# Kernel tuning notes

Measured on AMD Instinct MI355X. Metric: run time of the kernel, lower is better.

The kernel has to match this reference:

```python
import jax, jax.numpy as jnp
import numpy as np

N_QUBITS = 14
N_LAYERS = 3
BATCH = 256


def _apply_1q(state, U, q, n):
    # state: (B, 2^n) flat; apply 2x2 gate U on qubit q.
    # U: (2,2) shared or (B,2,2) per-sample.
    B = state.shape[0]
    s = state.reshape(B, 2 ** q, 2, 2 ** (n - 1 - q))
    if U.ndim == 3:
        s = jnp.einsum('bij,bajc->baic', U, s)
    else:
        s = jnp.einsum('ij,bajc->baic', U, s)
    return s.reshape(B, -1)


def _apply_cnot(state, c, t, n):
    # CNOT: |c, t> -> |c, t xor c>. Flip target axis on the control=1 block.
    B = state.shape[0]
    a, b = (c, t) if c < t else (t, c)
    s = state.reshape(B, 2 ** a, 2, 2 ** (b - a - 1), 2, 2 ** (n - 1 - b))
    c_ax = 2 if c < t else 4
    t_ax = 4 if c < t else 2
    s0 = jax.lax.index_in_dim(s, 0, axis=c_ax, keepdims=False)
    s1 = jax.lax.index_in_dim(s, 1, axis=c_ax, keepdims=False)
    t_ax2 = t_ax if t_ax < c_ax else t_ax - 1
    s1 = jnp.flip(s1, axis=t_ax2)
    s = jnp.stack([s0, s1], axis=c_ax)
    return s.reshape(B, -1)


def _circuit(x, weights, n, L):
    # angles constrained to (-pi, pi) as in the torch wrapper
    angles = jnp.tanh(x) * jnp.float32(np.pi)  # (B, n)
    B = x.shape[0]
    state = jnp.zeros((B, 2 ** n), jnp.complex64).at[:, 0].set(1.0)
    # AngleEmbedding with RY rotations (per-sample gate matrices)
    for q in range(n):
        th = angles[:, q] * 0.5
        c, s = jnp.cos(th), jnp.sin(th)
        U = jnp.stack([jnp.stack([c, -s], -1), jnp.stack([s, c], -1)], -2)
        state = _apply_1q(state, U.astype(jnp.complex64), q, n)
    # BasicEntanglerLayers: per layer, RX(w) on each wire then CNOT ring
    for l in range(L):
        for q in range(n):
            th = weights[l, q] * 0.5
            c = jnp.cos(th).astype(jnp.complex64)
            s = jnp.sin(th).astype(jnp.complex64)
            mis = jnp.complex64(-1j) * s
            U = jnp.stack([jnp.stack([c, mis]), jnp.stack([mis, c])])
            state = _apply_1q(state, U, q, n)
        num_cnots = n if n > 2 else (1 if n == 2 else 0)
        for q in range(num_cnots):
            state = _apply_cnot(state, q, (q + 1) % n, n)
    # <Z_q> = P(q=0) - P(q=1)
    p = (jnp.abs(state) ** 2).reshape((B,) + (2,) * n)  # float32 probs
    expvals = []
    for q in range(n):
        pq = jnp.sum(p, axis=tuple(a for a in range(1, n + 1) if a != q + 1))
        expvals.append(pq[:, 0] - pq[:, 1])
    return jnp.stack(expvals, axis=-1)  # (B, n)


def setup_inputs() -> dict:
    key = jax.random.key(0)
    kx, kw = jax.random.split(key)
    x = jax.random.normal(kx, (BATCH, N_QUBITS), jnp.float32)
    # TorchLayer default init for BasicEntanglerLayers: uniform in [0, 2*pi)
    weights = jax.random.uniform(kw, (N_LAYERS, N_QUBITS), jnp.float32, 0.0, 2.0 * np.pi)
    return {"x": x, "weights": weights}


def reference(x, weights):
    return _circuit(x, weights, N_QUBITS, N_LAYERS)
```

## Files before the change

kernel.cpp:

```cpp
#include <hip/hip_runtime.h>
#include <math.h>

#define NQ 14
#define DIM (1 << NQ)
#define NT 512
#define TA 32
#define NW (NT / 64)
#define PDIM (DIM + DIM / 32)

template <int J> struct IC { static constexpr int v = J; };
template <int N, typename F>
__device__ __forceinline__ void sfor(F&& f) {
    if constexpr (N > 0) { sfor<N - 1>(f); f(IC<N - 1>{}); }
}

typedef float cf2 __attribute__((ext_vector_type(2)));

__device__ __forceinline__ cf2 pk_mul_s_swapneg(cf2 cs, cf2 a) {
    cf2 t;
    asm("v_pk_mul_f32 %0, %1, %2 op_sel:[1,1] op_sel_hi:[1,0] neg_hi:[0,1]"
        : "=v"(t) : "v"(cs), "v"(a));
    return t;
}
__device__ __forceinline__ cf2 pk_fma_c(cf2 cs, cf2 a, cf2 b) {
    cf2 d;
    asm("v_pk_fma_f32 %0, %1, %2, %3 op_sel:[0,0,0] op_sel_hi:[0,1,1]"
        : "=v"(d) : "v"(cs), "v"(a), "v"(b));
    return d;
}

struct St {
    cf2 a0, a1, a2, a3, a4, a5, a6, a7, a8, a9, a10, a11, a12, a13, a14, a15,
        a16, a17, a18, a19, a20, a21, a22, a23, a24, a25, a26, a27, a28, a29, a30, a31;
};
template <int J> __device__ __forceinline__ cf2& amp(St& s);
#define AMP_GET(J) template <> __device__ __forceinline__ cf2& amp<J>(St& s) { return s.a##J; }
AMP_GET(0)  AMP_GET(1)  AMP_GET(2)  AMP_GET(3)  AMP_GET(4)  AMP_GET(5)  AMP_GET(6)  AMP_GET(7)
AMP_GET(8)  AMP_GET(9)  AMP_GET(10) AMP_GET(11) AMP_GET(12) AMP_GET(13) AMP_GET(14) AMP_GET(15)
AMP_GET(16) AMP_GET(17) AMP_GET(18) AMP_GET(19) AMP_GET(20) AMP_GET(21) AMP_GET(22) AMP_GET(23)
AMP_GET(24) AMP_GET(25) AMP_GET(26) AMP_GET(27) AMP_GET(28) AMP_GET(29) AMP_GET(30) AMP_GET(31)

__host__ __device__ constexpr int pad(int idx) { return idx + (idx >> 5); }

template <int P0, int P1, int P2, int P3, int P4>
struct Tile5 {
    static constexpr int PMASK = (1 << P0) | (1 << P1) | (1 << P2) | (1 << P3) | (1 << P4);
    static __device__ __forceinline__ int base_idx(int t) {
        int idx = 0, tb = 0;
#pragma unroll
        for (int p = 0; p < NQ; ++p)
            if (!((PMASK >> p) & 1)) { idx |= ((t >> tb) & 1) << p; ++tb; }
        return idx;
    }
    static constexpr int off(int j) {
        return ((j & 1) << P0) | (((j >> 1) & 1) << P1) | (((j >> 2) & 1) << P2) |
               (((j >> 3) & 1) << P3) | (((j >> 4) & 1) << P4);
    }
    static constexpr int poff(int j) { return pad(off(j)); }
};
template <int P0, int P1, int P2, int P3, int P4,
          int Q0, int Q1, int Q2, int Q3, int Q4, int Q5, int Q6, int Q7, int Q8>
struct Tile5Q {
    static __device__ __forceinline__ int base_idx(int t) {
        return (((t >> 0) & 1) << Q0) | (((t >> 1) & 1) << Q1) | (((t >> 2) & 1) << Q2) |
               (((t >> 3) & 1) << Q3) | (((t >> 4) & 1) << Q4) | (((t >> 5) & 1) << Q5) |
               (((t >> 6) & 1) << Q6) | (((t >> 7) & 1) << Q7) | (((t >> 8) & 1) << Q8);
    }
    static constexpr int off(int j) {
        return ((j & 1) << P0) | (((j >> 1) & 1) << P1) | (((j >> 2) & 1) << P2) |
               (((j >> 3) & 1) << P3) | (((j >> 4) & 1) << P4);
    }
    static constexpr int poff(int j) { return pad(off(j)); }
};

using TT1 = Tile5<9, 10, 11, 12, 13>;
using TT2Q = Tile5Q<4, 5, 6, 7, 8,  9, 0, 1, 2, 3, 10, 11, 12, 13>;
using TT3 = Tile5<13, 0, 1, 2, 3>;

template <class T>
__device__ __forceinline__ void load_tile_fold(const cf2* s, int pbLo, int pbHi, St& st) {
    sfor<TA>([&](auto jc) {
        constexpr int j0 = decltype(jc)::v;
        constexpr int j = (j0 >> 1) | ((j0 & 1) << 4);
        amp<j>(st) = s[((j & 16) ? pbHi : pbLo) + T::poff(j)];
    });
}
template <class T, int HI>
__device__ __forceinline__ void store_half(cf2* s, int pb, St& st) {
    sfor<TA>([&](auto jc) {
        constexpr int j = decltype(jc)::v;
        if constexpr ((j >> 4) == HI) s[pb + T::poff(j)] = amp<j>(st);
    });
}

template <int LB>
__device__ __forceinline__ void g_rx(St& st, cf2 cs) {
    sfor<TA>([&](auto jc) {
        constexpr int j = decltype(jc)::v;
        if constexpr (!(j & (1 << LB))) {
            constexpr int k = j | (1 << LB);
            cf2 aj = amp<j>(st), ak = amp<k>(st);
            amp<j>(st) = pk_fma_c(cs, aj, pk_mul_s_swapneg(cs, ak));
            amp<k>(st) = pk_fma_c(cs, ak, pk_mul_s_swapneg(cs, aj));
        }
    });
}
template <int LB, int HI>
__device__ __forceinline__ void g_rx_h(St& st, cf2 cs) {
    sfor<TA>([&](auto jc) {
        constexpr int j = decltype(jc)::v;
        if constexpr (!(j & (1 << LB)) && ((j >> 4) == HI)) {
            constexpr int k = j | (1 << LB);
            cf2 aj = amp<j>(st), ak = amp<k>(st);
            amp<j>(st) = pk_fma_c(cs, aj, pk_mul_s_swapneg(cs, ak));
            amp<k>(st) = pk_fma_c(cs, ak, pk_mul_s_swapneg(cs, aj));
        }
    });
}
template <int CTRL>
__device__ __forceinline__ void g_rx_lane_dpp(St& st, cf2 cs) {
    sfor<TA>([&](auto jc) {
        constexpr int j = decltype(jc)::v;
        cf2 a = amp<j>(st);
        int px = __builtin_amdgcn_update_dpp(__float_as_int(a.x), __float_as_int(a.x),
                                             CTRL, 0xF, 0xF, false);
        int py = __builtin_amdgcn_update_dpp(__float_as_int(a.y), __float_as_int(a.y),
                                             CTRL, 0xF, 0xF, false);
        cf2 p; p.x = __int_as_float(px); p.y = __int_as_float(py);
        amp<j>(st) = pk_fma_c(cs, a, pk_mul_s_swapneg(cs, p));
    });
}
template <int LC, int LT, int HI>
__device__ __forceinline__ void g_cnot_h(St& st) {
    sfor<TA>([&](auto jc) {
        constexpr int j = decltype(jc)::v;
        if constexpr (((j >> LC) & 1) && !((j >> LT) & 1) && ((j >> 4) == HI)) {
            constexpr int k = j | (1 << LT);
            cf2 t = amp<j>(st);
            amp<j>(st) = amp<k>(st);
            amp<k>(st) = t;
        }
    });
}

__device__ __forceinline__ cf2 cmul(cf2 a, cf2 b) {
    cf2 r; r.x = a.x * b.x - a.y * b.y; r.y = a.x * b.y + a.y * b.x; return r;
}
__device__ __forceinline__ cf2 v_of(cf2 ry, cf2 rx, int b) {
    cf2 r;
    r.x = b ? rx.x * ry.y : rx.x * ry.x;
    r.y = b ? -(rx.y * ry.x) : -(rx.y * ry.y);
    return r;
}

template <int CTRL, int RM>
__device__ __forceinline__ float dpp_add_step(float v) {
    int t = __builtin_amdgcn_update_dpp(0, __float_as_int(v), CTRL, RM, 0xF, true);
    return v + __int_as_float(t);
}
__device__ __forceinline__ float wave_red(float v) {
    v = dpp_add_step<0x111, 0xF>(v);
    v = dpp_add_step<0x112, 0xF>(v);
    v = dpp_add_step<0x114, 0xF>(v);
    v = dpp_add_step<0x118, 0xF>(v);
    v = dpp_add_step<0x142, 0xA>(v);
    v = dpp_add_step<0x143, 0xC>(v);
    return v;
}

__global__ void __launch_bounds__(NT) qsim_kernel(const float* __restrict__ x,
                                                  const float* __restrict__ w,
                                                  float* __restrict__ out) {
    __shared__ cf2 sSt[PDIM];
    __shared__ cf2 sCS[56];
    __shared__ float sRed[NW][NQ];

    const int tid = threadIdx.x;
    const int b = blockIdx.x;

    if (tid < 56) {
        float f;
        if (tid < 14) {
            float v = x[b * NQ + tid];
            float e = __builtin_amdgcn_exp2f(v * 2.8853900817779268f);
            float t = fmaf(-2.f, __builtin_amdgcn_rcpf(e + 1.f), 1.f);
            f = t * 0.25f;
        } else {
            f = w[tid - 14] * 0.07957747154594767f;
        }
        cf2 v2; v2.x = __builtin_amdgcn_cosf(f); v2.y = __builtin_amdgcn_sinf(f);
        sCS[tid] = v2;
    }

    const int pbT1 = pad(TT1::base_idx(tid));
    const int pbT2 = pad(TT2Q::base_idx(tid));
    const int pbT3 = pad(TT3::base_idx(tid));
    const int d2 = (tid & 1) ? 264 : 0;
    const int pbT2lo = pbT2 + d2, pbT2hi = pbT2 - d2;
    const int d3 = (tid & 1) ? 8 : 0;
    const int pbT3lo = pbT3 + d3, pbT3hi = pbT3 - d3;

    __syncthreads();

    St st;

    {
        const int t0 = tid & 1,        t1 = (tid >> 1) & 1, t2 = (tid >> 2) & 1,
                  t3 = (tid >> 3) & 1, t4 = (tid >> 4) & 1, t5 = (tid >> 5) & 1,
                  t6 = (tid >> 6) & 1, t7 = (tid >> 7) & 1, t8 = (tid >> 8) & 1;
        const int b6 = t7 ^ t8, b7 = t6 ^ t7, b8 = t5 ^ t6, b9 = t4 ^ t5;
        const int b10 = t3 ^ t4, b11 = t2 ^ t3, b12 = t1 ^ t2, b13 = t0 ^ t1;
        cf2 Pref = v_of(sCS[6], sCS[20], b6);
        Pref = cmul(Pref, v_of(sCS[7],  sCS[21], b7));
        Pref = cmul(Pref, v_of(sCS[8],  sCS[22], b8));
        Pref = cmul(Pref, v_of(sCS[9],  sCS[23], b9));
        Pref = cmul(Pref, v_of(sCS[10], sCS[24], b10));
        Pref = cmul(Pref, v_of(sCS[11], sCS[25], b11));
        Pref = cmul(Pref, v_of(sCS[12], sCS[26], b12));
        Pref = cmul(Pref, v_of(sCS[13], sCS[27], b13));
        cf2 w0[2] = { v_of(sCS[0], sCS[14], t0),     v_of(sCS[0], sCS[14], 1 ^ t0) };
        cf2 w1[2] = { v_of(sCS[1], sCS[15], t0),     v_of(sCS[1], sCS[15], 1 ^ t0) };
        cf2 v2[2] = { v_of(sCS[2], sCS[16], 0),      v_of(sCS[2], sCS[16], 1) };
        cf2 v3[2] = { v_of(sCS[3], sCS[17], 0),      v_of(sCS[3], sCS[17], 1) };
        cf2 v4[2] = { v_of(sCS[4], sCS[18], 0),      v_of(sCS[4], sCS[18], 1) };
        cf2 w5[2] = { v_of(sCS[5], sCS[19], t8),     v_of(sCS[5], sCS[19], 1 ^ t8) };
        cf2 u[4] = { cmul(v4[0], w5[0]), cmul(v4[1], w5[1]),
                     cmul(v4[1], w5[0]), cmul(v4[0], w5[1]) };
        cf2 tA[2], tB[4], tC[8], tD[16];
        sfor<2>([&](auto ic) {
            constexpr int i = decltype(ic)::v;
            tA[i] = cmul(Pref, w0[i]);
        });
        sfor<4>([&](auto ic) {
            constexpr int i = decltype(ic)::v;
            constexpr int j4 = i >> 1, j3 = i & 1;
            tB[i] = cmul(tA[j4], w1[j3 ^ j4]);
        });
        sfor<8>([&](auto ic) {
            constexpr int i = decltype(ic)::v;
            constexpr int j3 = (i >> 1) & 1, j2 = i & 1;
            tC[i] = cmul(tB[i >> 1], v2[j2 ^ j3]);
        });
        sfor<16>([&](auto ic) {
            constexpr int i = decltype(ic)::v;
            constexpr int j2 = (i >> 1) & 1, j1 = i & 1;
            tD[i] = cmul(tC[i >> 1], v3[j1 ^ j2]);
        });
        sfor<TA>([&](auto jc) {
            constexpr int j = decltype(jc)::v;
            constexpr int j0 = j & 1, j1 = (j >> 1) & 1;
            amp<j>(st) = cmul(tD[j >> 1], u[(j1 << 1) | j0]);
        });

        g_rx<4>(st, sCS[28 + 0]);
        g_rx_h<3, 0>(st, sCS[28 + 1]); g_rx_h<2, 0>(st, sCS[28 + 2]);
        g_rx_h<1, 0>(st, sCS[28 + 3]); g_rx_h<0, 0>(st, sCS[28 + 4]);
        g_cnot_h<3, 2, 0>(st); g_cnot_h<2, 1, 0>(st); g_cnot_h<1, 0, 0>(st);
        g_rx_h<3, 0>(st, sCS[42 + 1]); g_rx_h<2, 0>(st, sCS[42 + 2]);
        g_rx_h<1, 0>(st, sCS[42 + 3]);
        store_half<TT1, 0>(sSt, pbT1, st);
        g_rx_h<3, 1>(st, sCS[28 + 1]); g_rx_h<2, 1>(st, sCS[28 + 2]);
        g_rx_h<1, 1>(st, sCS[28 + 3]); g_rx_h<0, 1>(st, sCS[28 + 4]);
        g_cnot_h<4, 3, 1>(st); g_cnot_h<3, 2, 1>(st); g_cnot_h<2, 1, 1>(st); g_cnot_h<1, 0, 1>(st);
        g_rx_h<3, 1>(st, sCS[42 + 1]); g_rx_h<2, 1>(st, sCS[42 + 2]);
        g_rx_h<1, 1>(st, sCS[42 + 3]);
        store_half<TT1, 1>(sSt, pbT1, st);
    }
    __syncthreads();

    {
        cf2 c5 = sCS[28 + 5], c6 = sCS[28 + 6], c7 = sCS[28 + 7];
        cf2 c8 = sCS[28 + 8], c9 = sCS[28 + 9];
        cf2 e4 = sCS[42 + 4], e5 = sCS[42 + 5], e6 = sCS[42 + 6];
        cf2 e7 = sCS[42 + 7], e8 = sCS[42 + 8];
        load_tile_fold<TT2Q>(sSt, pbT2lo, pbT2hi, st);
        g_rx<4>(st, c5);
        g_rx_lane_dpp<0xB1>(st, e4);
        g_rx_h<3,0>(st, c6); g_rx_h<2,0>(st, c7); g_rx_h<1,0>(st, c8); g_rx_h<0,0>(st, c9);
        g_cnot_h<3,2,0>(st); g_cnot_h<2,1,0>(st); g_cnot_h<1,0,0>(st);
        g_rx_h<3,1>(st, c6); g_rx_h<2,1>(st, c7); g_rx_h<1,1>(st, c8); g_rx_h<0,1>(st, c9);
        g_cnot_h<4,3,1>(st); g_cnot_h<3,2,1>(st); g_cnot_h<2,1,1>(st); g_cnot_h<1,0,1>(st);
        g_rx<4>(st, e5);
        g_rx_h<3,0>(st, e6); g_rx_h<2,0>(st, e7); g_rx_h<1,0>(st, e8);
        store_half<TT2Q, 0>(sSt, pbT2, st);
        g_rx_h<3,1>(st, e6); g_rx_h<2,1>(st, e7); g_rx_h<1,1>(st, e8);
        store_half<TT2Q, 1>(sSt, pbT2, st);
    }
    __syncthreads();

    {
        cf2 cA = sCS[28 + 10], cB = sCS[28 + 11], cC = sCS[28 + 12], cD = sCS[28 + 13];
        cf2 eA = sCS[42 + 10], eB = sCS[42 + 11], eC = sCS[42 + 12], eD = sCS[42 + 13];
        cf2 e9 = sCS[42 + 9],  e0 = sCS[42 + 0];
        load_tile_fold<TT3>(sSt, pbT3lo, pbT3hi, st);
        g_rx<4>(st, cA);
        g_rx_lane_dpp<0xB1>(st, e9);
        g_rx_h<3,0>(st, cB); g_rx_h<2,0>(st, cC); g_rx_h<1,0>(st, cD);
        g_cnot_h<3,2,0>(st); g_cnot_h<2,1,0>(st); g_cnot_h<1,0,0>(st);
        g_rx_h<3,1>(st, cB); g_rx_h<2,1>(st, cC); g_rx_h<1,1>(st, cD);
        g_cnot_h<4,3,1>(st); g_cnot_h<3,2,1>(st); g_cnot_h<2,1,1>(st); g_cnot_h<1,0,1>(st);
        g_rx<4>(st, eA);
        g_rx_h<3,0>(st, eB); g_rx_h<2,0>(st, eC); g_rx_h<1,0>(st, eD); g_rx_h<0,0>(st, e0);
        g_rx_h<3,1>(st, eB); g_rx_h<2,1>(st, eC); g_rx_h<1,1>(st, eD); g_rx_h<0,1>(st, e0);
    }

    {
        float Aa = 0.f, Ab = 0.f, Ac = 0.f, Ad = 0.f, Ae = 0.f, Af = 0.f;
        sfor<TA>([&](auto jc) {
            constexpr int j = decltype(jc)::v;
            cf2 v = amp<j>(st);
            float pj = v.x * v.x + v.y * v.y;
            constexpr int j0 = j & 1, j1 = (j >> 1) & 1, j2 = (j >> 2) & 1,
                          j3 = (j >> 3) & 1, j4 = (j >> 4) & 1;
            constexpr int sa = j0;
            constexpr int sb = j0 ^ j4;
            constexpr int sc = sb ^ j3;
            constexpr int sd = sc ^ j2;
            constexpr int se = sd ^ j1;
            constexpr int sf = se ^ j0;
            Aa += sa ? -pj : pj;
            Ab += sb ? -pj : pj;
            Ac += sc ? -pj : pj;
            Ad += sd ? -pj : pj;
            Ae += se ? -pj : pj;
            Af += sf ? -pj : pj;
        });
        const int t0 = tid & 1,        t1 = (tid >> 1) & 1, t2 = (tid >> 2) & 1,
                  t3 = (tid >> 3) & 1, t4 = (tid >> 4) & 1, t5 = (tid >> 5) & 1,
                  t6 = (tid >> 6) & 1, t7 = (tid >> 7) & 1, t8 = (tid >> 8) & 1;
        const int L4 = t5, L5 = L4 ^ t4, L6 = L5 ^ t3;
        const int L7 = L6 ^ t2, L8 = L7 ^ t1, L9 = L8 ^ t0;
        const int W1 = t8, W2 = W1 ^ t7, W3 = W2 ^ t6;

        float R0 = wave_red(Aa);
        float R4 = wave_red(L4 ? -Aa : Aa);
        float R5 = wave_red(L5 ? -Aa : Aa);
        float R6 = wave_red(L6 ? -Aa : Aa);
        float R7 = wave_red(L7 ? -Aa : Aa);
        float R8 = wave_red(L8 ? -Aa : Aa);
        float R9 = wave_red(L9 ? -Aa : Aa);
        float RB = wave_red(L9 ? -Ab : Ab);
        float RC = wave_red(L9 ? -Ac : Ac);
        float RD = wave_red(L9 ? -Ad : Ad);
        float RE = wave_red(L9 ? -Ae : Ae);
        float RF = wave_red(L9 ? -Af : Af);

        const int wv = tid >> 6, ln = tid & 63;
        if (ln == 63) {
            sRed[wv][0]  = W3 ? -RF : RF;
            sRed[wv][1]  = W1 ? -R0 : R0;
            sRed[wv][2]  = W2 ? -R0 : R0;
            sRed[wv][3]  = W3 ? -R0 : R0;
            sRed[wv][4]  = W3 ? -R4 : R4;
            sRed[wv][5]  = W3 ? -R5 : R5;
            sRed[wv][6]  = W3 ? -R6 : R6;
            sRed[wv][7]  = W3 ? -R7 : R7;
            sRed[wv][8]  = W3 ? -R8 : R8;
            sRed[wv][9]  = W3 ? -R9 : R9;
            sRed[wv][10] = W3 ? -RB : RB;
            sRed[wv][11] = W3 ? -RC : RC;
            sRed[wv][12] = W3 ? -RD : RD;
            sRed[wv][13] = W3 ? -RE : RE;
        }
        __syncthreads();
        if (tid < NQ) {
            float acc = 0.f;
#pragma unroll
            for (int k = 0; k < NW; ++k) acc += sRed[k][tid];
            out[b * NQ + tid] = acc;
        }
    }
}

extern "C" void kernel_launch(void* const* d_in, const int* in_sizes, int n_in,
                              void* d_out, int out_size, void* d_ws, size_t ws_size,
                              hipStream_t stream) {
    const float* x = (const float*)d_in[0];
    const float* w = (const float*)d_in[1];
    float* out = (float*)d_out;
    qsim_kernel<<<256, NT, 0, stream>>>(x, w, out);
}
```

Measured before the change: 67.87 us.

## Double threads per block with 16-amplitude register tiles and DPP cross-lane gates

Raises the block size from 512 to 1024 threads and halves each thread's register tile from 32 to 16 amplitudes. All three LDS tile layouts, the product-state initialisation and the reduction sign bookkeeping are redefined for the new split. More gates and CNOTs that now cross lanes are done with DPP lane swaps (quad_perm patterns) instead of in-register pairs, and the half-tile staging of the old version is dropped. The intent is more parallelism and lower register pressure per thread, at the cost of extra DPP traffic, more wave reductions per block and a larger block to synchronise.

```diff
diff --git a/kernel.cpp b/kernel.cpp
--- a/kernel.cpp
+++ b/kernel.cpp
@@ -3,8 +3,8 @@
 
 #define NQ 14
 #define DIM (1 << NQ)
-#define NT 512
-#define TA 32
+#define NT 1024
+#define TA 16
 #define NW (NT / 64)
 #define PDIM (DIM + DIM / 32)
 
@@ -30,66 +30,48 @@
 }
 
 struct St {
-    cf2 a0, a1, a2, a3, a4, a5, a6, a7, a8, a9, a10, a11, a12, a13, a14, a15,
-        a16, a17, a18, a19, a20, a21, a22, a23, a24, a25, a26, a27, a28, a29, a30, a31;
+    cf2 a0, a1, a2, a3, a4, a5, a6, a7, a8, a9, a10, a11, a12, a13, a14, a15;
 };
 template <int J> __device__ __forceinline__ cf2& amp(St& s);
 #define AMP_GET(J) template <> __device__ __forceinline__ cf2& amp<J>(St& s) { return s.a##J; }
 AMP_GET(0)  AMP_GET(1)  AMP_GET(2)  AMP_GET(3)  AMP_GET(4)  AMP_GET(5)  AMP_GET(6)  AMP_GET(7)
 AMP_GET(8)  AMP_GET(9)  AMP_GET(10) AMP_GET(11) AMP_GET(12) AMP_GET(13) AMP_GET(14) AMP_GET(15)
-AMP_GET(16) AMP_GET(17) AMP_GET(18) AMP_GET(19) AMP_GET(20) AMP_GET(21) AMP_GET(22) AMP_GET(23)
-AMP_GET(24) AMP_GET(25) AMP_GET(26) AMP_GET(27) AMP_GET(28) AMP_GET(29) AMP_GET(30) AMP_GET(31)
 
 __host__ __device__ constexpr int pad(int idx) { return idx + (idx >> 5); }
 
-template <int P0, int P1, int P2, int P3, int P4>
-struct Tile5 {
-    static constexpr int PMASK = (1 << P0) | (1 << P1) | (1 << P2) | (1 << P3) | (1 << P4);
-    static __device__ __forceinline__ int base_idx(int t) {
-        int idx = 0, tb = 0;
-#pragma unroll
-        for (int p = 0; p < NQ; ++p)
-            if (!((PMASK >> p) & 1)) { idx |= ((t >> tb) & 1) << p; ++tb; }
-        return idx;
-    }
-    static constexpr int off(int j) {
-        return ((j & 1) << P0) | (((j >> 1) & 1) << P1) | (((j >> 2) & 1) << P2) |
-               (((j >> 3) & 1) << P3) | (((j >> 4) & 1) << P4);
-    }
-    static constexpr int poff(int j) { return pad(off(j)); }
-};
-template <int P0, int P1, int P2, int P3, int P4,
-          int Q0, int Q1, int Q2, int Q3, int Q4, int Q5, int Q6, int Q7, int Q8>
-struct Tile5Q {
+template <int P0, int P1, int P2, int P3,
+          int Q0, int Q1, int Q2, int Q3, int Q4, int Q5, int Q6, int Q7, int Q8, int Q9>
+struct Tile4Q {
     static __device__ __forceinline__ int base_idx(int t) {
         return (((t >> 0) & 1) << Q0) | (((t >> 1) & 1) << Q1) | (((t >> 2) & 1) << Q2) |
                (((t >> 3) & 1) << Q3) | (((t >> 4) & 1) << Q4) | (((t >> 5) & 1) << Q5) |
-               (((t >> 6) & 1) << Q6) | (((t >> 7) & 1) << Q7) | (((t >> 8) & 1) << Q8);
+               (((t >> 6) & 1) << Q6) | (((t >> 7) & 1) << Q7) | (((t >> 8) & 1) << Q8) |
+               (((t >> 9) & 1) << Q9);
     }
     static constexpr int off(int j) {
         return ((j & 1) << P0) | (((j >> 1) & 1) << P1) | (((j >> 2) & 1) << P2) |
-               (((j >> 3) & 1) << P3) | (((j >> 4) & 1) << P4);
+               (((j >> 3) & 1) << P3);
     }
     static constexpr int poff(int j) { return pad(off(j)); }
 };
 
-using TT1 = Tile5<9, 10, 11, 12, 13>;
-using TT2Q = Tile5Q<4, 5, 6, 7, 8,  9, 0, 1, 2, 3, 10, 11, 12, 13>;
-using TT3 = Tile5<13, 0, 1, 2, 3>;
+using TP1 = Tile4Q<10, 11, 12, 13,  9, 8, 0, 1, 2, 3, 4, 5, 6, 7>;
+using TP2 = Tile4Q<4, 5, 6, 7,  3, 8, 0, 1, 2, 9, 10, 11, 12, 13>;
+using TP3 = Tile4Q<13, 0, 1, 2,  3, 4, 5, 6, 7, 8, 9, 10, 11, 12>;
 
 template <class T>
 __device__ __forceinline__ void load_tile_fold(const cf2* s, int pbLo, int pbHi, St& st) {
     sfor<TA>([&](auto jc) {
         constexpr int j0 = decltype(jc)::v;
-        constexpr int j = (j0 >> 1) | ((j0 & 1) << 4);
-        amp<j>(st) = s[((j & 16) ? pbHi : pbLo) + T::poff(j)];
-    });
-}
-template <class T, int HI>
-__device__ __forceinline__ void store_half(cf2* s, int pb, St& st) {
-    sfor<TA>([&](auto jc) {
-        constexpr int j = decltype(jc)::v;
-        if constexpr ((j >> 4) == HI) s[pb + T::poff(j)] = amp<j>(st);
+        constexpr int j = (j0 >> 1) | ((j0 & 1) << 3);
+        amp<j>(st) = s[((j & 8) ? pbHi : pbLo) + T::poff(j)];
+    });
+}
+template <class T>
+__device__ __forceinline__ void store_tile(cf2* s, int pb, St& st) {
+    sfor<TA>([&](auto jc) {
+        constexpr int j = decltype(jc)::v;
+        s[pb + T::poff(j)] = amp<j>(st);
     });
 }
 
@@ -98,18 +80,6 @@
     sfor<TA>([&](auto jc) {
         constexpr int j = decltype(jc)::v;
         if constexpr (!(j & (1 << LB))) {
-            constexpr int k = j | (1 << LB);
-            cf2 aj = amp<j>(st), ak = amp<k>(st);
-            amp<j>(st) = pk_fma_c(cs, aj, pk_mul_s_swapneg(cs, ak));
-            amp<k>(st) = pk_fma_c(cs, ak, pk_mul_s_swapneg(cs, aj));
-        }
-    });
-}
-template <int LB, int HI>
-__device__ __forceinline__ void g_rx_h(St& st, cf2 cs) {
-    sfor<TA>([&](auto jc) {
-        constexpr int j = decltype(jc)::v;
-        if constexpr (!(j & (1 << LB)) && ((j >> 4) == HI)) {
             constexpr int k = j | (1 << LB);
             cf2 aj = amp<j>(st), ak = amp<k>(st);
             amp<j>(st) = pk_fma_c(cs, aj, pk_mul_s_swapneg(cs, ak));
@@ -130,16 +100,44 @@
         amp<j>(st) = pk_fma_c(cs, a, pk_mul_s_swapneg(cs, p));
     });
 }
-template <int LC, int LT, int HI>
-__device__ __forceinline__ void g_cnot_h(St& st) {
-    sfor<TA>([&](auto jc) {
-        constexpr int j = decltype(jc)::v;
-        if constexpr (((j >> LC) & 1) && !((j >> LT) & 1) && ((j >> 4) == HI)) {
+template <int LC, int LT>
+__device__ __forceinline__ void g_cnot(St& st) {
+    sfor<TA>([&](auto jc) {
+        constexpr int j = decltype(jc)::v;
+        if constexpr (((j >> LC) & 1) && !((j >> LT) & 1)) {
             constexpr int k = j | (1 << LT);
             cf2 t = amp<j>(st);
             amp<j>(st) = amp<k>(st);
             amp<k>(st) = t;
         }
+    });
+}
+template <int CTRL, int CB>
+__device__ __forceinline__ void g_cnot_dppmov(St& st) {
+    sfor<TA>([&](auto jc) {
+        constexpr int j = decltype(jc)::v;
+        if constexpr ((j >> CB) & 1) {
+            cf2 a = amp<j>(st);
+            int px = __builtin_amdgcn_update_dpp(__float_as_int(a.x), __float_as_int(a.x),
+                                                 CTRL, 0xF, 0xF, false);
+            int py = __builtin_amdgcn_update_dpp(__float_as_int(a.y), __float_as_int(a.y),
+                                                 CTRL, 0xF, 0xF, false);
+            cf2 p; p.x = __int_as_float(px); p.y = __int_as_float(py);
+            amp<j>(st) = p;
+        }
+    });
+}
+template <int CTRL>
+__device__ __forceinline__ void g_cnot_cnd(St& st, bool ctrl) {
+    sfor<TA>([&](auto jc) {
+        constexpr int j = decltype(jc)::v;
+        cf2 a = amp<j>(st);
+        int px = __builtin_amdgcn_update_dpp(__float_as_int(a.x), __float_as_int(a.x),
+                                             CTRL, 0xF, 0xF, false);
+        int py = __builtin_amdgcn_update_dpp(__float_as_int(a.y), __float_as_int(a.y),
+                                             CTRL, 0xF, 0xF, false);
+        cf2 p; p.x = __int_as_float(px); p.y = __int_as_float(py);
+        amp<j>(st) = ctrl ? p : a;
     });
 }
 
@@ -192,13 +190,13 @@
         sCS[tid] = v2;
     }
 
-    const int pbT1 = pad(TT1::base_idx(tid));
-    const int pbT2 = pad(TT2Q::base_idx(tid));
-    const int pbT3 = pad(TT3::base_idx(tid));
-    const int d2 = (tid & 1) ? 264 : 0;
-    const int pbT2lo = pbT2 + d2, pbT2hi = pbT2 - d2;
-    const int d3 = (tid & 1) ? 8 : 0;
-    const int pbT3lo = pbT3 + d3, pbT3hi = pbT3 - d3;
+    const int pb1 = pad(TP1::base_idx(tid));
+    const int pb2 = pad(TP2::base_idx(tid));
+    const int pb3 = pad(TP3::base_idx(tid));
+    const int d2 = ((tid >> 1) & 1) ? 132 : 0;
+    const int pb2lo = pb2 + d2, pb2hi = pb2 - d2;
+    const int d3 = (tid & 1) ? 4 : 0;
+    const int pb3lo = pb3 + d3, pb3hi = pb3 - d3;
 
     __syncthreads();
 
@@ -207,160 +205,137 @@
     {
         const int t0 = tid & 1,        t1 = (tid >> 1) & 1, t2 = (tid >> 2) & 1,
                   t3 = (tid >> 3) & 1, t4 = (tid >> 4) & 1, t5 = (tid >> 5) & 1,
-                  t6 = (tid >> 6) & 1, t7 = (tid >> 7) & 1, t8 = (tid >> 8) & 1;
-        const int b6 = t7 ^ t8, b7 = t6 ^ t7, b8 = t5 ^ t6, b9 = t4 ^ t5;
-        const int b10 = t3 ^ t4, b11 = t2 ^ t3, b12 = t1 ^ t2, b13 = t0 ^ t1;
-        cf2 Pref = v_of(sCS[6], sCS[20], b6);
-        Pref = cmul(Pref, v_of(sCS[7],  sCS[21], b7));
-        Pref = cmul(Pref, v_of(sCS[8],  sCS[22], b8));
-        Pref = cmul(Pref, v_of(sCS[9],  sCS[23], b9));
-        Pref = cmul(Pref, v_of(sCS[10], sCS[24], b10));
-        Pref = cmul(Pref, v_of(sCS[11], sCS[25], b11));
-        Pref = cmul(Pref, v_of(sCS[12], sCS[26], b12));
-        Pref = cmul(Pref, v_of(sCS[13], sCS[27], b13));
-        cf2 w0[2] = { v_of(sCS[0], sCS[14], t0),     v_of(sCS[0], sCS[14], 1 ^ t0) };
-        cf2 w1[2] = { v_of(sCS[1], sCS[15], t0),     v_of(sCS[1], sCS[15], 1 ^ t0) };
-        cf2 v2[2] = { v_of(sCS[2], sCS[16], 0),      v_of(sCS[2], sCS[16], 1) };
-        cf2 v3[2] = { v_of(sCS[3], sCS[17], 0),      v_of(sCS[3], sCS[17], 1) };
-        cf2 v4[2] = { v_of(sCS[4], sCS[18], 0),      v_of(sCS[4], sCS[18], 1) };
-        cf2 w5[2] = { v_of(sCS[5], sCS[19], t8),     v_of(sCS[5], sCS[19], 1 ^ t8) };
-        cf2 u[4] = { cmul(v4[0], w5[0]), cmul(v4[1], w5[1]),
-                     cmul(v4[1], w5[0]), cmul(v4[0], w5[1]) };
-        cf2 tA[2], tB[4], tC[8], tD[16];
+                  t6 = (tid >> 6) & 1, t7 = (tid >> 7) & 1, t8 = (tid >> 8) & 1,
+                  t9 = (tid >> 9) & 1;
+        cf2 Pref = v_of(sCS[5], sCS[19], t1 ^ t0);
+        Pref = cmul(Pref, v_of(sCS[6],  sCS[20], t9 ^ t1));
+        Pref = cmul(Pref, v_of(sCS[7],  sCS[21], t8 ^ t9));
+        Pref = cmul(Pref, v_of(sCS[8],  sCS[22], t7 ^ t8));
+        Pref = cmul(Pref, v_of(sCS[9],  sCS[23], t6 ^ t7));
+        Pref = cmul(Pref, v_of(sCS[10], sCS[24], t5 ^ t6));
+        Pref = cmul(Pref, v_of(sCS[11], sCS[25], t4 ^ t5));
+        Pref = cmul(Pref, v_of(sCS[12], sCS[26], t3 ^ t4));
+        Pref = cmul(Pref, v_of(sCS[13], sCS[27], t2 ^ t3));
+        cf2 w0[2] = { v_of(sCS[0], sCS[14], t2), v_of(sCS[0], sCS[14], 1 ^ t2) };
+        cf2 w1[2] = { v_of(sCS[1], sCS[15], t2), v_of(sCS[1], sCS[15], 1 ^ t2) };
+        cf2 v2a[2] = { v_of(sCS[2], sCS[16], 0), v_of(sCS[2], sCS[16], 1) };
+        cf2 v3a[2] = { v_of(sCS[3], sCS[17], 0), v_of(sCS[3], sCS[17], 1) };
+        cf2 w4[2] = { v_of(sCS[4], sCS[18], t0), v_of(sCS[4], sCS[18], 1 ^ t0) };
+        cf2 u[4] = { cmul(v3a[0], w4[0]), cmul(v3a[1], w4[1]),
+                     cmul(v3a[1], w4[0]), cmul(v3a[0], w4[1]) };
+        cf2 tA[2], tB[4], tC[8];
         sfor<2>([&](auto ic) {
             constexpr int i = decltype(ic)::v;
             tA[i] = cmul(Pref, w0[i]);
         });
         sfor<4>([&](auto ic) {
             constexpr int i = decltype(ic)::v;
-            constexpr int j4 = i >> 1, j3 = i & 1;
-            tB[i] = cmul(tA[j4], w1[j3 ^ j4]);
+            constexpr int j3b = i >> 1, j2b = i & 1;
+            tB[i] = cmul(tA[j3b], w1[j2b ^ j3b]);
         });
         sfor<8>([&](auto ic) {
             constexpr int i = decltype(ic)::v;
-            constexpr int j3 = (i >> 1) & 1, j2 = i & 1;
-            tC[i] = cmul(tB[i >> 1], v2[j2 ^ j3]);
-        });
-        sfor<16>([&](auto ic) {
-            constexpr int i = decltype(ic)::v;
-            constexpr int j2 = (i >> 1) & 1, j1 = i & 1;
-            tD[i] = cmul(tC[i >> 1], v3[j1 ^ j2]);
+            constexpr int j2b = (i >> 1) & 1, j1b = i & 1;
+            tC[i] = cmul(tB[i >> 1], v2a[j1b ^ j2b]);
         });
         sfor<TA>([&](auto jc) {
             constexpr int j = decltype(jc)::v;
-            constexpr int j0 = j & 1, j1 = (j >> 1) & 1;
-            amp<j>(st) = cmul(tD[j >> 1], u[(j1 << 1) | j0]);
-        });
-
-        g_rx<4>(st, sCS[28 + 0]);
-        g_rx_h<3, 0>(st, sCS[28 + 1]); g_rx_h<2, 0>(st, sCS[28 + 2]);
-        g_rx_h<1, 0>(st, sCS[28 + 3]); g_rx_h<0, 0>(st, sCS[28 + 4]);
-        g_cnot_h<3, 2, 0>(st); g_cnot_h<2, 1, 0>(st); g_cnot_h<1, 0, 0>(st);
-        g_rx_h<3, 0>(st, sCS[42 + 1]); g_rx_h<2, 0>(st, sCS[42 + 2]);
-        g_rx_h<1, 0>(st, sCS[42 + 3]);
-        store_half<TT1, 0>(sSt, pbT1, st);
-        g_rx_h<3, 1>(st, sCS[28 + 1]); g_rx_h<2, 1>(st, sCS[28 + 2]);
-        g_rx_h<1, 1>(st, sCS[28 + 3]); g_rx_h<0, 1>(st, sCS[28 + 4]);
-        g_cnot_h<4, 3, 1>(st); g_cnot_h<3, 2, 1>(st); g_cnot_h<2, 1, 1>(st); g_cnot_h<1, 0, 1>(st);
-        g_rx_h<3, 1>(st, sCS[42 + 1]); g_rx_h<2, 1>(st, sCS[42 + 2]);
-        g_rx_h<1, 1>(st, sCS[42 + 3]);
-        store_half<TT1, 1>(sSt, pbT1, st);
+            amp<j>(st) = cmul(tC[j >> 1], u[j & 3]);
+        });
+
+        g_rx<3>(st, sCS[28 + 0]); g_rx<2>(st, sCS[28 + 1]);
+        g_rx<1>(st, sCS[28 + 2]); g_rx<0>(st, sCS[28 + 3]);
+        g_rx_lane_dpp<0xB1>(st, sCS[28 + 4]);
+        g_rx_lane_dpp<0x4E>(st, sCS[28 + 5]);
+        g_cnot<3, 2>(st); g_cnot<2, 1>(st); g_cnot<1, 0>(st);
+        g_cnot_dppmov<0xB1, 0>(st);
+        g_cnot_cnd<0x4E>(st, (bool)(tid & 1));
+        g_rx<2>(st, sCS[42 + 1]); g_rx<1>(st, sCS[42 + 2]); g_rx<0>(st, sCS[42 + 3]);
+        g_rx_lane_dpp<0xB1>(st, sCS[42 + 4]);
+        store_tile<TP1>(sSt, pb1, st);
     }
     __syncthreads();
 
     {
-        cf2 c5 = sCS[28 + 5], c6 = sCS[28 + 6], c7 = sCS[28 + 7];
-        cf2 c8 = sCS[28 + 8], c9 = sCS[28 + 9];
-        cf2 e4 = sCS[42 + 4], e5 = sCS[42 + 5], e6 = sCS[42 + 6];
-        cf2 e7 = sCS[42 + 7], e8 = sCS[42 + 8];
-        load_tile_fold<TT2Q>(sSt, pbT2lo, pbT2hi, st);
-        g_rx<4>(st, c5);
-        g_rx_lane_dpp<0xB1>(st, e4);
-        g_rx_h<3,0>(st, c6); g_rx_h<2,0>(st, c7); g_rx_h<1,0>(st, c8); g_rx_h<0,0>(st, c9);
-        g_cnot_h<3,2,0>(st); g_cnot_h<2,1,0>(st); g_cnot_h<1,0,0>(st);
-        g_rx_h<3,1>(st, c6); g_rx_h<2,1>(st, c7); g_rx_h<1,1>(st, c8); g_rx_h<0,1>(st, c9);
-        g_cnot_h<4,3,1>(st); g_cnot_h<3,2,1>(st); g_cnot_h<2,1,1>(st); g_cnot_h<1,0,1>(st);
-        g_rx<4>(st, e5);
-        g_rx_h<3,0>(st, e6); g_rx_h<2,0>(st, e7); g_rx_h<1,0>(st, e8);
-        store_half<TT2Q, 0>(sSt, pbT2, st);
-        g_rx_h<3,1>(st, e6); g_rx_h<2,1>(st, e7); g_rx_h<1,1>(st, e8);
-        store_half<TT2Q, 1>(sSt, pbT2, st);
+        load_tile_fold<TP2>(sSt, pb2lo, pb2hi, st);
+        g_rx<3>(st, sCS[28 + 6]); g_rx<2>(st, sCS[28 + 7]);
+        g_rx<1>(st, sCS[28 + 8]); g_rx<0>(st, sCS[28 + 9]);
+        g_rx_lane_dpp<0xB1>(st, sCS[28 + 10]);
+        g_rx_lane_dpp<0x4E>(st, sCS[42 + 5]);
+        g_cnot<3, 2>(st); g_cnot<2, 1>(st); g_cnot<1, 0>(st);
+        g_cnot_dppmov<0xB1, 0>(st);
+        g_rx<3>(st, sCS[42 + 6]); g_rx<2>(st, sCS[42 + 7]);
+        g_rx<1>(st, sCS[42 + 8]); g_rx<0>(st, sCS[42 + 9]);
+        store_tile<TP2>(sSt, pb2, st);
     }
     __syncthreads();
 
     {
-        cf2 cA = sCS[28 + 10], cB = sCS[28 + 11], cC = sCS[28 + 12], cD = sCS[28 + 13];
-        cf2 eA = sCS[42 + 10], eB = sCS[42 + 11], eC = sCS[42 + 12], eD = sCS[42 + 13];
-        cf2 e9 = sCS[42 + 9],  e0 = sCS[42 + 0];
-        load_tile_fold<TT3>(sSt, pbT3lo, pbT3hi, st);
-        g_rx<4>(st, cA);
-        g_rx_lane_dpp<0xB1>(st, e9);
-        g_rx_h<3,0>(st, cB); g_rx_h<2,0>(st, cC); g_rx_h<1,0>(st, cD);
-        g_cnot_h<3,2,0>(st); g_cnot_h<2,1,0>(st); g_cnot_h<1,0,0>(st);
-        g_rx_h<3,1>(st, cB); g_rx_h<2,1>(st, cC); g_rx_h<1,1>(st, cD);
-        g_cnot_h<4,3,1>(st); g_cnot_h<3,2,1>(st); g_cnot_h<2,1,1>(st); g_cnot_h<1,0,1>(st);
-        g_rx<4>(st, eA);
-        g_rx_h<3,0>(st, eB); g_rx_h<2,0>(st, eC); g_rx_h<1,0>(st, eD); g_rx_h<0,0>(st, e0);
-        g_rx_h<3,1>(st, eB); g_rx_h<2,1>(st, eC); g_rx_h<1,1>(st, eD); g_rx_h<0,1>(st, e0);
+        load_tile_fold<TP3>(sSt, pb3lo, pb3hi, st);
+        g_rx<3>(st, sCS[28 + 11]); g_rx<2>(st, sCS[28 + 12]); g_rx<1>(st, sCS[28 + 13]);
+        g_rx_lane_dpp<0xB1>(st, sCS[42 + 10]);
+        g_cnot<3, 2>(st);
+        g_cnot<2, 1>(st);
+        g_cnot<1, 0>(st);
+        g_rx<3>(st, sCS[42 + 11]); g_rx<2>(st, sCS[42 + 12]);
+        g_rx<1>(st, sCS[42 + 13]); g_rx<0>(st, sCS[42 + 0]);
     }
 
     {
-        float Aa = 0.f, Ab = 0.f, Ac = 0.f, Ad = 0.f, Ae = 0.f, Af = 0.f;
+        float A0 = 0.f, A1 = 0.f, A2 = 0.f, A3 = 0.f, A4 = 0.f;
         sfor<TA>([&](auto jc) {
             constexpr int j = decltype(jc)::v;
             cf2 v = amp<j>(st);
             float pj = v.x * v.x + v.y * v.y;
             constexpr int j0 = j & 1, j1 = (j >> 1) & 1, j2 = (j >> 2) & 1,
-                          j3 = (j >> 3) & 1, j4 = (j >> 4) & 1;
-            constexpr int sa = j0;
-            constexpr int sb = j0 ^ j4;
-            constexpr int sc = sb ^ j3;
-            constexpr int sd = sc ^ j2;
-            constexpr int se = sd ^ j1;
-            constexpr int sf = se ^ j0;
-            Aa += sa ? -pj : pj;
-            Ab += sb ? -pj : pj;
-            Ac += sc ? -pj : pj;
-            Ad += sd ? -pj : pj;
-            Ae += se ? -pj : pj;
-            Af += sf ? -pj : pj;
+                          j3 = (j >> 3) & 1;
+            constexpr int s0 = j3 ^ j2 ^ j1;
+            constexpr int s1 = j0;
+            constexpr int s2 = j0 ^ j3;
+            constexpr int s3 = s2 ^ j2;
+            constexpr int s4 = s3 ^ j1;
+            A0 += s0 ? -pj : pj;
+            A1 += s1 ? -pj : pj;
+            A2 += s2 ? -pj : pj;
+            A3 += s3 ? -pj : pj;
+            A4 += s4 ? -pj : pj;
         });
         const int t0 = tid & 1,        t1 = (tid >> 1) & 1, t2 = (tid >> 2) & 1,
                   t3 = (tid >> 3) & 1, t4 = (tid >> 4) & 1, t5 = (tid >> 5) & 1,
-                  t6 = (tid >> 6) & 1, t7 = (tid >> 7) & 1, t8 = (tid >> 8) & 1;
-        const int L4 = t5, L5 = L4 ^ t4, L6 = L5 ^ t3;
-        const int L7 = L6 ^ t2, L8 = L7 ^ t1, L9 = L8 ^ t0;
-        const int W1 = t8, W2 = W1 ^ t7, W3 = W2 ^ t6;
-
-        float R0 = wave_red(Aa);
-        float R4 = wave_red(L4 ? -Aa : Aa);
-        float R5 = wave_red(L5 ? -Aa : Aa);
-        float R6 = wave_red(L6 ? -Aa : Aa);
-        float R7 = wave_red(L7 ? -Aa : Aa);
-        float R8 = wave_red(L8 ? -Aa : Aa);
-        float R9 = wave_red(L9 ? -Aa : Aa);
-        float RB = wave_red(L9 ? -Ab : Ab);
-        float RC = wave_red(L9 ? -Ac : Ac);
-        float RD = wave_red(L9 ? -Ad : Ad);
-        float RE = wave_red(L9 ? -Ae : Ae);
-        float RF = wave_red(L9 ? -Af : Af);
+                  t6 = (tid >> 6) & 1, t7 = (tid >> 7) & 1, t8 = (tid >> 8) & 1,
+                  t9 = (tid >> 9) & 1;
+        const int L5 = t5, L6 = L5 ^ t4, L7 = L6 ^ t3, L8 = L7 ^ t2, L9 = L8 ^ t1;
+        const int LA = L9 ^ t0;
+        const int W1 = t9, W2 = W1 ^ t8, W3 = W2 ^ t7, W4 = W3 ^ t6;
+
+        float RZ0 = wave_red(LA ? -A0 : A0);
+        float R14 = wave_red(A1);
+        float R5  = wave_red(L5 ? -A1 : A1);
+        float R6  = wave_red(L6 ? -A1 : A1);
+        float R7  = wave_red(L7 ? -A1 : A1);
+        float R8  = wave_red(L8 ? -A1 : A1);
+        float R9  = wave_red(L9 ? -A1 : A1);
+        float R10 = wave_red(LA ? -A1 : A1);
+        float R11 = wave_red(LA ? -A2 : A2);
+        float R12 = wave_red(LA ? -A3 : A3);
+        float R13 = wave_red(LA ? -A4 : A4);
 
         const int wv = tid >> 6, ln = tid & 63;
         if (ln == 63) {
-            sRed[wv][0]  = W3 ? -RF : RF;
-            sRed[wv][1]  = W1 ? -R0 : R0;
-            sRed[wv][2]  = W2 ? -R0 : R0;
-            sRed[wv][3]  = W3 ? -R0 : R0;
-            sRed[wv][4]  = W3 ? -R4 : R4;
-            sRed[wv][5]  = W3 ? -R5 : R5;
-            sRed[wv][6]  = W3 ? -R6 : R6;
-            sRed[wv][7]  = W3 ? -R7 : R7;
-            sRed[wv][8]  = W3 ? -R8 : R8;
-            sRed[wv][9]  = W3 ? -R9 : R9;
-            sRed[wv][10] = W3 ? -RB : RB;
-            sRed[wv][11] = W3 ? -RC : RC;
-            sRed[wv][12] = W3 ? -RD : RD;
-            sRed[wv][13] = W3 ? -RE : RE;
+            sRed[wv][0]  = W4 ? -RZ0 : RZ0;
+            sRed[wv][1]  = W1 ? -R14 : R14;
+            sRed[wv][2]  = W2 ? -R14 : R14;
+            sRed[wv][3]  = W3 ? -R14 : R14;
+            sRed[wv][4]  = W4 ? -R14 : R14;
+            sRed[wv][5]  = W4 ? -R5  : R5;
+            sRed[wv][6]  = W4 ? -R6  : R6;
+            sRed[wv][7]  = W4 ? -R7  : R7;
+            sRed[wv][8]  = W4 ? -R8  : R8;
+            sRed[wv][9]  = W4 ? -R9  : R9;
+            sRed[wv][10] = W4 ? -R10 : R10;
+            sRed[wv][11] = W4 ? -R11 : R11;
+            sRed[wv][12] = W4 ? -R12 : R12;
+            sRed[wv][13] = W4 ? -R13 : R13;
         }
         __syncthreads();
         if (tid < NQ) {
```

New measurement: 71.71 us. +5.7%, slower.
